# Kernel optimization log

Measured on AMD Instinct MI355X. Metric: run time of the kernel, lower is better.

The kernel has to match this reference:

```python
import jax, jax.numpy as jnp
import numpy as np

HEADS = 16
DK = 64
THETA = 10000.0


def _rope(x, cos, sin):
    # x: (B, S, H, dk) -> rotate consecutive pairs as complex numbers
    xr = x.reshape(*x.shape[:-1], -1, 2)
    a, b = xr[..., 0], xr[..., 1]
    c = cos[None, :, None, :]  # (1, S, 1, dk//2)
    s = sin[None, :, None, :]
    out = jnp.stack([a * c - b * s, a * s + b * c], axis=-1)
    return out.reshape(x.shape)


def setup_inputs() -> dict:
    key = jax.random.key(0)
    ks = jax.random.split(key, 5)
    B, S, D = 4, 2048, 1024
    x = jax.random.normal(ks[0], (B, S, D), dtype=jnp.float32)
    scale = 1.0 / np.sqrt(D).astype(np.float32)
    Wq = jax.random.normal(ks[1], (D, D), dtype=jnp.float32) * scale
    Wk = jax.random.normal(ks[2], (D, D), dtype=jnp.float32) * scale
    Wv = jax.random.normal(ks[3], (D, D), dtype=jnp.float32) * scale
    Wo = jax.random.normal(ks[4], (D, D), dtype=jnp.float32) * scale
    # freqs_cis = exp(i * t * theta^{-2j/dk}), represented as cos/sin
    t = jnp.arange(S, dtype=jnp.float32)
    inv_freq = 1.0 / (THETA ** (jnp.arange(0, DK, 2, dtype=jnp.float32) / DK))
    ang = t[:, None] * inv_freq[None, :]  # (S, dk//2)
    return {"in_features": x, "freqs_cos": jnp.cos(ang), "freqs_sin": jnp.sin(ang),
            "Wq": Wq, "Wk": Wk, "Wv": Wv, "Wo": Wo}


def reference(in_features, freqs_cos, freqs_sin, Wq, Wk, Wv, Wo):
    B, S, D = in_features.shape
    H = HEADS
    dk = D // H
    # Linear projections (torch Linear: x @ W.T)
    q = (in_features @ Wq.T).reshape(B, S, H, dk)
    k = (in_features @ Wk.T).reshape(B, S, H, dk)
    v = (in_features @ Wv.T).reshape(B, S, H, dk)
    q = _rope(q, freqs_cos, freqs_sin)
    k = _rope(k, freqs_cos, freqs_sin)
    scale = 1.0 / jnp.sqrt(jnp.asarray(dk, dtype=q.dtype))
    scores = jnp.einsum("bqhd,bkhd->bhqk", q, k) * scale
    mask = jnp.tril(jnp.ones((S, S), dtype=bool))
    scores = jnp.where(mask[None, None, :, :], scores, -jnp.inf)
    attn = jax.nn.softmax(scores, axis=-1)
    out = jnp.einsum("bhqk,bkhd->bqhd", attn, v).reshape(B, S, D)
    return out @ Wo.T
```

## Files before the change

kernel.cpp:

```cpp
#include <hip/hip_runtime.h>
#include <hip/hip_bf16.h>

typedef __attribute__((ext_vector_type(8))) __bf16 bf16x8;
typedef __attribute__((ext_vector_type(4))) __bf16 bf16x4;
typedef __attribute__((ext_vector_type(4))) float f32x4;
typedef __attribute__((ext_vector_type(2))) unsigned int u32x2;

static __device__ __forceinline__ f32x4 mfma_bf16(bf16x8 a, bf16x8 b, f32x4 c) {
  return __builtin_amdgcn_mfma_f32_16x16x32_bf16(a, b, c, 0, 0, 0);
}

static __device__ __forceinline__ void gload_lds16(const void* g, void* l) {
  __builtin_amdgcn_global_load_lds(
      (__attribute__((address_space(1))) unsigned int*)g,
      (__attribute__((address_space(3))) unsigned int*)l, 16, 0, 0);
}

static __device__ __forceinline__ unsigned int cvt_pk_bf16(float lo, float hi) {
  unsigned int r;
  asm volatile("v_cvt_pk_bf16_f32 %0, %1, %2" : "=v"(r) : "v"(lo), "v"(hi));
  return r;
}

__global__ void cvt_bf16(const float* __restrict__ in, __bf16* __restrict__ out, int n4) {
  int i = blockIdx.x * blockDim.x + threadIdx.x;
  if (i >= n4) return;
  f32x4 v = ((const f32x4*)in)[i];
  bf16x4 o;
#pragma unroll
  for (int k = 0; k < 4; ++k) o[k] = (__bf16)v[k];
  ((bf16x4*)out)[i] = o;
}

__global__ void cvt_w4(const float* __restrict__ w0, const float* __restrict__ w1,
                       const float* __restrict__ w2, const float* __restrict__ w3,
                       __bf16* __restrict__ o0, __bf16* __restrict__ o1,
                       __bf16* __restrict__ o2, __bf16* __restrict__ o3) {
  const float* in; __bf16* out;
  switch (blockIdx.y) {
    case 0: in = w0; out = o0; break;
    case 1: in = w1; out = o1; break;
    case 2: in = w2; out = o2; break;
    default: in = w3; out = o3; break;
  }
  int i = blockIdx.x * blockDim.x + threadIdx.x;
  f32x4 v = ((const f32x4*)in)[i];
  bf16x4 o;
#pragma unroll
  for (int k = 0; k < 4; ++k) o[k] = (__bf16)v[k];
  ((bf16x4*)out)[i] = o;
}

template <int MODE>
__global__ __launch_bounds__(512, 1)
void gemm256(const __bf16* __restrict__ A, const __bf16* __restrict__ W,
             void* __restrict__ outp,
             const float* __restrict__ fcos, const float* __restrict__ fsin) {
  constexpr int K = 1024;
  constexpr int NT = K / 64;
  extern __shared__ __align__(16) __bf16 dynlds[];
  __bf16* Al = dynlds;
  __bf16* Bl = dynlds + 49152;

  const int t = threadIdx.x;
  const int lane = t & 63, wave = t >> 6;
  const int g = lane >> 4, ln = lane & 15;
  const int wm = wave >> 1, wn = wave & 1;
  const int lin = blockIdx.x + blockIdx.y * 8;
  const int bm = (lin & 7) + 8 * ((lin >> 3) & 3);
  const int bn = lin >> 5;

  f32x4 acc[4][4] = {};

  const int srow8 = t >> 3;
  const int scole = (((t & 7) ^ ((t >> 3) & 7)) << 3);
  const __bf16* Ag = A + (size_t)(bm * 256 + srow8) * K + scole;
  const __bf16* Wg = W + (size_t)(bn * 128 + srow8) * K + scole;

#define ISSUE_A(kt, slot)                                                   \
  {                                                                         \
    const int k0 = (kt) * 64;                                               \
    __bf16* d = Al + (slot) * 16384 + t * 8;                                \
    gload_lds16(Ag + k0, d);                                                \
    gload_lds16(Ag + (size_t)64 * K + k0, d + 4096);                        \
    gload_lds16(Ag + (size_t)128 * K + k0, d + 8192);                       \
    gload_lds16(Ag + (size_t)192 * K + k0, d + 12288);                      \
  }
#define ISSUE_B(kt, slot)                                                   \
  {                                                                         \
    const int k0 = (kt) * 64;                                               \
    __bf16* d = Bl + (slot) * 8192 + t * 8;                                 \
    gload_lds16(Wg + k0, d);                                                \
    gload_lds16(Wg + (size_t)64 * K + k0, d + 4096);                        \
  }

  const int axr = ln & 7;
  int aoff[4], boff[4];
#pragma unroll
  for (int i = 0; i < 4; ++i) aoff[i] = (wm * 64 + i * 16 + ln) * 64;
#pragma unroll
  for (int j = 0; j < 4; ++j) boff[j] = (wn * 64 + j * 16 + ln) * 64;

  ISSUE_B(0, 0);
  ISSUE_A(0, 0);
  ISSUE_A(1, 1);
  asm volatile("s_waitcnt vmcnt(4)" ::: "memory");
  __builtin_amdgcn_s_barrier();

  int sa = 0;
  for (int tt = 0; tt < NT; ++tt) {
    const __bf16* Ab = Al + sa * 16384;
    const __bf16* Bb = Bl + (tt & 1) * 8192;
    bf16x8 af[4], bf[4];

#pragma unroll
    for (int i = 0; i < 4; ++i)
      af[i] = *(const bf16x8*)(Ab + aoff[i] + ((g ^ axr) << 3));
#pragma unroll
    for (int j = 0; j < 4; ++j)
      bf[j] = *(const bf16x8*)(Bb + boff[j] + ((g ^ axr) << 3));
    if (tt + 1 < NT) ISSUE_B(tt + 1, (tt + 1) & 1);
    if (tt + 2 < NT) ISSUE_A(tt + 2, sa == 0 ? 2 : sa - 1);
    __builtin_amdgcn_s_barrier();
    asm volatile("s_waitcnt lgkmcnt(0)" ::: "memory");
    __builtin_amdgcn_sched_barrier(0);
    __builtin_amdgcn_s_setprio(1);
#pragma unroll
    for (int i = 0; i < 4; ++i)
#pragma unroll
      for (int j = 0; j < 4; ++j)
        acc[i][j] = mfma_bf16(af[i], bf[j], acc[i][j]);
    __builtin_amdgcn_s_setprio(0);
    __builtin_amdgcn_s_barrier();

#pragma unroll
    for (int i = 0; i < 4; ++i)
      af[i] = *(const bf16x8*)(Ab + aoff[i] + (((4 | g) ^ axr) << 3));
#pragma unroll
    for (int j = 0; j < 4; ++j)
      bf[j] = *(const bf16x8*)(Bb + boff[j] + (((4 | g) ^ axr) << 3));
    if (tt < NT - 2) { asm volatile("s_waitcnt vmcnt(4)" ::: "memory"); }
    else             { asm volatile("s_waitcnt vmcnt(0)" ::: "memory"); }
    __builtin_amdgcn_s_barrier();
    asm volatile("s_waitcnt lgkmcnt(0)" ::: "memory");
    __builtin_amdgcn_sched_barrier(0);
    __builtin_amdgcn_s_setprio(1);
#pragma unroll
    for (int i = 0; i < 4; ++i)
#pragma unroll
      for (int j = 0; j < 4; ++j)
        acc[i][j] = mfma_bf16(af[i], bf[j], acc[i][j]);
    __builtin_amdgcn_s_setprio(0);
    __builtin_amdgcn_s_barrier();

    sa = (sa == 2) ? 0 : sa + 1;
  }
#undef ISSUE_A
#undef ISSUE_B

#pragma unroll
  for (int i = 0; i < 4; ++i) {
    const int mbase = bm * 256 + wm * 64 + i * 16 + g * 4;
#pragma unroll
    for (int j = 0; j < 4; ++j) {
      const int col = bn * 128 + wn * 64 + j * 16 + ln;
      if constexpr (MODE == 0 || MODE == 1) {
        const int fi = (col & 63) >> 1;
        const bool odd = (col & 1) != 0;
        __bf16* O = (__bf16*)outp;
#pragma unroll
        for (int r = 0; r < 4; ++r) {
          const int row = mbase + r;
          const int tok = row & 2047;
          const float cs = fcos[tok * 32 + fi];
          const float sn = fsin[tok * 32 + fi];
          const float own = acc[i][j][r];
          const float oth = __shfl_xor(own, 1);
          float val = own * cs + (odd ? oth * sn : -oth * sn);
          if constexpr (MODE == 0) val *= 0.1803368802f;
          O[(size_t)row * 1024 + col] = (__bf16)val;
        }
      } else if constexpr (MODE == 2) {
        __bf16* O = (__bf16*)outp;
        const int bb = mbase >> 11;
        const int tok = mbase & 2047;
        bf16x4 pk;
#pragma unroll
        for (int r = 0; r < 4; ++r) pk[r] = (__bf16)acc[i][j][r];
        *(bf16x4*)(O + ((size_t)(bb * 1024 + col)) * 2048 + tok) = pk;
      } else {
        float* O = (float*)outp;
#pragma unroll
        for (int r = 0; r < 4; ++r)
          O[(size_t)(mbase + r) * 1024 + col] = acc[i][j][r];
      }
    }
  }
}

__global__ __launch_bounds__(512, 4)
void attn_fwd(const __bf16* __restrict__ Q, const __bf16* __restrict__ Kk,
              const __bf16* __restrict__ Vt, __bf16* __restrict__ U) {
  constexpr int S = 2048;
  __shared__ __align__(16) __bf16 Klds[2][2 * 64 * 32];
  __shared__ __align__(16) __bf16 Vlds[2][2 * 64 * 32];
  __shared__ __align__(16) unsigned int Plds[8][16 * 36];

  const int t = threadIdx.x;
  const int lane = t & 63, wave = t >> 6;
  const int g = lane >> 4, ln = lane & 15;
  const int lin = blockIdx.x + blockIdx.y * 8;
  const int bh = (lin & 7) * 8 + ((lin >> 3) & 7);
  const int qt = lin >> 6;
  const int b = bh >> 4, h = bh & 15;
  const int q0s[2] = {qt * 128, (15 - qt) * 128};
  const int nts[2] = {2 * qt + 2, 32 - 2 * qt};

  bf16x8 qf[2][2];
#pragma unroll
  for (int s2 = 0; s2 < 2; ++s2) {
    const __bf16* Qb = Q + ((size_t)(b * S + q0s[s2] + wave * 16 + ln)) * 1024 + h * 64;
    qf[s2][0] = *(const bf16x8*)(Qb + g * 8);
    qf[s2][1] = *(const bf16x8*)(Qb + 32 + g * 8);
  }

  f32x4 o[2][4] = {};
  float mrow[2], lrow[2];
#pragma unroll
  for (int s2 = 0; s2 < 2; ++s2) { mrow[s2] = -3.0e38f; lrow[s2] = 0.f; }

  const int half = t >> 8;
  const int srow = (t >> 2) & 63;
  const int scol = (t & 3) * 8;
  const __bf16* Kg = Kk + ((size_t)(b * S + srow)) * 1024 + h * 64 + half * 32 + scol;
  const __bf16* Vg = Vt + ((size_t)(b * 1024 + h * 64 + srow)) * 2048 + half * 32 + scol;
  const int nt = nts[1];

  gload_lds16(Kg, (__bf16*)Klds[0] + t * 8);
  gload_lds16(Vg, (__bf16*)Vlds[0] + t * 8);
  __syncthreads();

  for (int kt = 0; kt < nt; ++kt) {
    const int cur = kt & 1;
    if (kt + 1 < nt) {
      const size_t kv1 = (size_t)(kt + 1) * 64;
      gload_lds16(Kg + kv1 * 1024, (__bf16*)Klds[cur ^ 1] + t * 8);
      gload_lds16(Vg + kv1, (__bf16*)Vlds[cur ^ 1] + t * 8);
    }
    const int kv0 = kt * 64;

#pragma unroll
    for (int s2 = 0; s2 < 2; ++s2) {
      if (kt >= nts[s2]) continue;

      f32x4 sa[4] = {};
      __builtin_amdgcn_s_setprio(1);
#pragma unroll
      for (int s = 0; s < 2; ++s) {
#pragma unroll
        for (int c = 0; c < 4; ++c) {
          bf16x8 kf = *(const bf16x8*)(Klds[cur] + s * 2048 + (c * 16 + ln) * 32 + g * 8);
          sa[c] = mfma_bf16(kf, qf[s2][s], sa[c]);
        }
      }
      __builtin_amdgcn_s_setprio(0);

      const int rfbase = q0s[s2] + wave * 16;
      const int rq = rfbase + ln;
      if (kv0 + 63 > rfbase) {
#pragma unroll
        for (int c = 0; c < 4; ++c)
#pragma unroll
          for (int r = 0; r < 4; ++r)
            if (kv0 + c * 16 + g * 4 + r > rq) sa[c][r] = -1e30f;
      }

      const float a0 = fmaxf(fmaxf(sa[0][0], sa[0][1]), sa[0][2]);
      const float a1 = fmaxf(fmaxf(sa[0][3], sa[1][0]), sa[1][1]);
      const float a2 = fmaxf(fmaxf(sa[1][2], sa[1][3]), sa[2][0]);
      const float a3 = fmaxf(fmaxf(sa[2][1], sa[2][2]), sa[2][3]);
      const float a4 = fmaxf(fmaxf(sa[3][0], sa[3][1]), sa[3][2]);
      const float b0 = fmaxf(fmaxf(a0, a1), a2);
      const float b1 = fmaxf(fmaxf(a3, a4), sa[3][3]);
      float pm = fmaxf(b0, b1);

      if (__any(pm > mrow[s2] + 8.f)) {
        pm = fmaxf(pm, __shfl_xor(pm, 16));
        pm = fmaxf(pm, __shfl_xor(pm, 32));
        const float mn = fmaxf(mrow[s2], pm);
        const float alpha = exp2f(mrow[s2] - mn);
        mrow[s2] = mn;
        lrow[s2] *= alpha;
#pragma unroll
        for (int c2 = 0; c2 < 4; ++c2)
#pragma unroll
          for (int r = 0; r < 4; ++r) o[s2][c2][r] *= alpha;
      }

      float p[4][4];
#pragma unroll
      for (int c = 0; c < 4; ++c)
#pragma unroll
        for (int r = 0; r < 4; ++r) p[c][r] = exp2f(sa[c][r] - mrow[s2]);

      float ts[8];
#pragma unroll
      for (int i = 0; i < 8; ++i) ts[i] = p[i >> 2][i & 3] + p[2 + (i >> 2)][i & 3];
#pragma unroll
      for (int st = 4; st >= 1; st >>= 1)
#pragma unroll
        for (int i = 0; i < st; ++i) ts[i] += ts[i + st];
      float rs = ts[0];
      rs += __shfl_xor(rs, 16);
      rs += __shfl_xor(rs, 32);
      lrow[s2] += rs;

      unsigned int* Pw = Plds[wave] + ln * 36;
#pragma unroll
      for (int c = 0; c < 4; ++c) {
        u32x2 w;
        w[0] = cvt_pk_bf16(p[c][0], p[c][1]);
        w[1] = cvt_pk_bf16(p[c][2], p[c][3]);
        *(u32x2*)(Pw + 8 * c + 2 * g) = w;
      }

      __builtin_amdgcn_s_setprio(1);
#pragma unroll
      for (int sh = 0; sh < 2; ++sh) {
        bf16x8 pb = *(const bf16x8*)((const __bf16*)(Plds[wave]) + ln * 72 + sh * 32 + g * 8);
#pragma unroll
        for (int c2 = 0; c2 < 4; ++c2) {
          bf16x8 vf = *(const bf16x8*)(Vlds[cur] + sh * 2048 + (c2 * 16 + ln) * 32 + g * 8);
          o[s2][c2] = mfma_bf16(vf, pb, o[s2][c2]);
        }
      }
      __builtin_amdgcn_s_setprio(0);
    }
    __syncthreads();
  }

#pragma unroll
  for (int s2 = 0; s2 < 2; ++s2) {
    const float rl = 1.0f / lrow[s2];
    __bf16* Ub = U + ((size_t)(b * S + q0s[s2] + wave * 16 + ln)) * 1024 + h * 64;
#pragma unroll
    for (int c2 = 0; c2 < 4; ++c2) {
      bf16x4 pk4;
#pragma unroll
      for (int r = 0; r < 4; ++r) pk4[r] = (__bf16)(o[s2][c2][r] * rl);
      *(bf16x4*)(Ub + 16 * c2 + 4 * g) = pk4;
    }
  }
}

extern "C" void kernel_launch(void* const* d_in, const int* in_sizes, int n_in,
                              void* d_out, int out_size, void* d_ws, size_t ws_size,
                              hipStream_t stream) {
  const float* x    = (const float*)d_in[0];
  const float* fcos = (const float*)d_in[1];
  const float* fsin = (const float*)d_in[2];
  const float* Wq   = (const float*)d_in[3];
  const float* Wk   = (const float*)d_in[4];
  const float* Wv   = (const float*)d_in[5];
  const float* Wo   = (const float*)d_in[6];

  char* ws = (char*)d_ws;
  __bf16* xb  = (__bf16*)(ws);
  __bf16* Wqb = (__bf16*)(ws + (16u << 20));
  __bf16* Wkb = (__bf16*)(ws + (18u << 20));
  __bf16* Wvb = (__bf16*)(ws + (20u << 20));
  __bf16* Wob = (__bf16*)(ws + (22u << 20));
  __bf16* Qb  = (__bf16*)(ws + (24u << 20));
  __bf16* Kb  = (__bf16*)(ws + (40u << 20));
  __bf16* Vtb = (__bf16*)(ws + (56u << 20));
  __bf16* Ub  = xb;

  cvt_bf16<<<8192, 256, 0, stream>>>(x, xb, 8192 * 1024 / 4);
  cvt_w4<<<dim3(1024, 4), 256, 0, stream>>>(Wq, Wk, Wv, Wo, Wqb, Wkb, Wvb, Wob);

  dim3 gg(8, 32);
  const size_t lds = 131072;
  gemm256<0><<<gg, 512, lds, stream>>>(xb, Wqb, Qb,  fcos, fsin);
  gemm256<1><<<gg, 512, lds, stream>>>(xb, Wkb, Kb,  fcos, fsin);
  gemm256<2><<<gg, 512, lds, stream>>>(xb, Wvb, Vtb, nullptr, nullptr);
  attn_fwd<<<dim3(8, 64), 512, 0, stream>>>(Qb, Kb, Vtb, Ub);
  gemm256<3><<<gg, 512, lds, stream>>>(Ub, Wob, d_out, nullptr, nullptr);
}
```

Baseline: 187.3 us.

## Merge Q/K/V projection GEMMs into one launch and interleave attention score MFMAs

Replaces three separate projection GEMM launches with one 768-block grid that picks Wq/Wk/Wv per block, so the grid fills the GPU better and launch gaps and tails are removed. In attention, the two query sub-tiles now share each K fragment load for their QK MFMAs, and softmax/PV is factored into a helper with separate P buffers per sub-tile. The cost is runtime branching on mode in the epilogue and doubled P LDS, which may affect occupancy or register pressure.

```diff
diff --git a/kernel.cpp b/kernel.cpp
--- a/kernel.cpp
+++ b/kernel.cpp
@@ -51,32 +51,6 @@
   ((bf16x4*)out)[i] = o;
 }
 
-template <int MODE>
-__global__ __launch_bounds__(512, 1)
-void gemm256(const __bf16* __restrict__ A, const __bf16* __restrict__ W,
-             void* __restrict__ outp,
-             const float* __restrict__ fcos, const float* __restrict__ fsin) {
-  constexpr int K = 1024;
-  constexpr int NT = K / 64;
-  extern __shared__ __align__(16) __bf16 dynlds[];
-  __bf16* Al = dynlds;
-  __bf16* Bl = dynlds + 49152;
-
-  const int t = threadIdx.x;
-  const int lane = t & 63, wave = t >> 6;
-  const int g = lane >> 4, ln = lane & 15;
-  const int wm = wave >> 1, wn = wave & 1;
-  const int lin = blockIdx.x + blockIdx.y * 8;
-  const int bm = (lin & 7) + 8 * ((lin >> 3) & 3);
-  const int bn = lin >> 5;
-
-  f32x4 acc[4][4] = {};
-
-  const int srow8 = t >> 3;
-  const int scole = (((t & 7) ^ ((t >> 3) & 7)) << 3);
-  const __bf16* Ag = A + (size_t)(bm * 256 + srow8) * K + scole;
-  const __bf16* Wg = W + (size_t)(bn * 128 + srow8) * K + scole;
-
 #define ISSUE_A(kt, slot)                                                   \
   {                                                                         \
     const int k0 = (kt) * 64;                                               \
@@ -94,69 +68,82 @@
     gload_lds16(Wg + (size_t)64 * K + k0, d + 4096);                        \
   }
 
-  const int axr = ln & 7;
-  int aoff[4], boff[4];
-#pragma unroll
-  for (int i = 0; i < 4; ++i) aoff[i] = (wm * 64 + i * 16 + ln) * 64;
-#pragma unroll
-  for (int j = 0; j < 4; ++j) boff[j] = (wn * 64 + j * 16 + ln) * 64;
-
-  ISSUE_B(0, 0);
-  ISSUE_A(0, 0);
-  ISSUE_A(1, 1);
-  asm volatile("s_waitcnt vmcnt(4)" ::: "memory");
-  __builtin_amdgcn_s_barrier();
-
-  int sa = 0;
-  for (int tt = 0; tt < NT; ++tt) {
-    const __bf16* Ab = Al + sa * 16384;
-    const __bf16* Bb = Bl + (tt & 1) * 8192;
-    bf16x8 af[4], bf[4];
-
-#pragma unroll
-    for (int i = 0; i < 4; ++i)
-      af[i] = *(const bf16x8*)(Ab + aoff[i] + ((g ^ axr) << 3));
-#pragma unroll
-    for (int j = 0; j < 4; ++j)
-      bf[j] = *(const bf16x8*)(Bb + boff[j] + ((g ^ axr) << 3));
-    if (tt + 1 < NT) ISSUE_B(tt + 1, (tt + 1) & 1);
-    if (tt + 2 < NT) ISSUE_A(tt + 2, sa == 0 ? 2 : sa - 1);
-    __builtin_amdgcn_s_barrier();
-    asm volatile("s_waitcnt lgkmcnt(0)" ::: "memory");
-    __builtin_amdgcn_sched_barrier(0);
-    __builtin_amdgcn_s_setprio(1);
-#pragma unroll
-    for (int i = 0; i < 4; ++i)
-#pragma unroll
-      for (int j = 0; j < 4; ++j)
-        acc[i][j] = mfma_bf16(af[i], bf[j], acc[i][j]);
-    __builtin_amdgcn_s_setprio(0);
-    __builtin_amdgcn_s_barrier();
-
-#pragma unroll
-    for (int i = 0; i < 4; ++i)
-      af[i] = *(const bf16x8*)(Ab + aoff[i] + (((4 | g) ^ axr) << 3));
-#pragma unroll
-    for (int j = 0; j < 4; ++j)
-      bf[j] = *(const bf16x8*)(Bb + boff[j] + (((4 | g) ^ axr) << 3));
-    if (tt < NT - 2) { asm volatile("s_waitcnt vmcnt(4)" ::: "memory"); }
-    else             { asm volatile("s_waitcnt vmcnt(0)" ::: "memory"); }
-    __builtin_amdgcn_s_barrier();
-    asm volatile("s_waitcnt lgkmcnt(0)" ::: "memory");
-    __builtin_amdgcn_sched_barrier(0);
-    __builtin_amdgcn_s_setprio(1);
-#pragma unroll
-    for (int i = 0; i < 4; ++i)
-#pragma unroll
-      for (int j = 0; j < 4; ++j)
-        acc[i][j] = mfma_bf16(af[i], bf[j], acc[i][j]);
-    __builtin_amdgcn_s_setprio(0);
-    __builtin_amdgcn_s_barrier();
-
-    sa = (sa == 2) ? 0 : sa + 1;
-  }
-#undef ISSUE_A
-#undef ISSUE_B
+#define GEMM_PIPELINE                                                       \
+  constexpr int K = 1024;                                                   \
+  constexpr int NT = K / 64;                                                \
+  extern __shared__ __align__(16) __bf16 dynlds[];                          \
+  __bf16* Al = dynlds;                                                      \
+  __bf16* Bl = dynlds + 49152;                                              \
+  const int t = threadIdx.x;                                                \
+  const int lane = t & 63, wave = t >> 6;                                   \
+  const int g = lane >> 4, ln = lane & 15;                                  \
+  const int wm = wave >> 1, wn = wave & 1;                                  \
+  f32x4 acc[4][4] = {};                                                     \
+  const int srow8 = t >> 3;                                                 \
+  const int scole = (((t & 7) ^ ((t >> 3) & 7)) << 3);                      \
+  const __bf16* Ag = A + (size_t)(bm * 256 + srow8) * K + scole;            \
+  const __bf16* Wg = W + (size_t)(bn * 128 + srow8) * K + scole;            \
+  const int axr = ln & 7;                                                   \
+  int aoff[4], boff[4];                                                     \
+  _Pragma("unroll") for (int i = 0; i < 4; ++i)                             \
+    aoff[i] = (wm * 64 + i * 16 + ln) * 64;                                 \
+  _Pragma("unroll") for (int j = 0; j < 4; ++j)                             \
+    boff[j] = (wn * 64 + j * 16 + ln) * 64;                                 \
+  ISSUE_B(0, 0); ISSUE_A(0, 0); ISSUE_A(1, 1);                              \
+  asm volatile("s_waitcnt vmcnt(4)" ::: "memory");                          \
+  __builtin_amdgcn_s_barrier();                                             \
+  int sa = 0;                                                               \
+  for (int tt = 0; tt < NT; ++tt) {                                         \
+    const __bf16* Ab = Al + sa * 16384;                                     \
+    const __bf16* Bb = Bl + (tt & 1) * 8192;                                \
+    bf16x8 af[4], bf[4];                                                    \
+    _Pragma("unroll") for (int i = 0; i < 4; ++i)                           \
+      af[i] = *(const bf16x8*)(Ab + aoff[i] + ((g ^ axr) << 3));            \
+    _Pragma("unroll") for (int j = 0; j < 4; ++j)                           \
+      bf[j] = *(const bf16x8*)(Bb + boff[j] + ((g ^ axr) << 3));            \
+    if (tt + 1 < NT) ISSUE_B(tt + 1, (tt + 1) & 1);                         \
+    if (tt + 2 < NT) ISSUE_A(tt + 2, sa == 0 ? 2 : sa - 1);                 \
+    __builtin_amdgcn_s_barrier();                                           \
+    asm volatile("s_waitcnt lgkmcnt(0)" ::: "memory");                      \
+    __builtin_amdgcn_sched_barrier(0);                                      \
+    __builtin_amdgcn_s_setprio(1);                                          \
+    _Pragma("unroll") for (int i = 0; i < 4; ++i)                           \
+      _Pragma("unroll") for (int j = 0; j < 4; ++j)                         \
+        acc[i][j] = mfma_bf16(af[i], bf[j], acc[i][j]);                     \
+    __builtin_amdgcn_s_setprio(0);                                          \
+    __builtin_amdgcn_s_barrier();                                           \
+    _Pragma("unroll") for (int i = 0; i < 4; ++i)                           \
+      af[i] = *(const bf16x8*)(Ab + aoff[i] + (((4 | g) ^ axr) << 3));      \
+    _Pragma("unroll") for (int j = 0; j < 4; ++j)                           \
+      bf[j] = *(const bf16x8*)(Bb + boff[j] + (((4 | g) ^ axr) << 3));      \
+    if (tt < NT - 2) { asm volatile("s_waitcnt vmcnt(4)" ::: "memory"); }   \
+    else             { asm volatile("s_waitcnt vmcnt(0)" ::: "memory"); }   \
+    __builtin_amdgcn_s_barrier();                                           \
+    asm volatile("s_waitcnt lgkmcnt(0)" ::: "memory");                      \
+    __builtin_amdgcn_sched_barrier(0);                                      \
+    __builtin_amdgcn_s_setprio(1);                                          \
+    _Pragma("unroll") for (int i = 0; i < 4; ++i)                           \
+      _Pragma("unroll") for (int j = 0; j < 4; ++j)                         \
+        acc[i][j] = mfma_bf16(af[i], bf[j], acc[i][j]);                     \
+    __builtin_amdgcn_s_setprio(0);                                          \
+    __builtin_amdgcn_s_barrier();                                           \
+    sa = (sa == 2) ? 0 : sa + 1;                                            \
+  }
+
+__global__ __launch_bounds__(512, 1)
+void gemm_qkv(const __bf16* __restrict__ A,
+              const __bf16* __restrict__ Wqp, const __bf16* __restrict__ Wkp,
+              const __bf16* __restrict__ Wvp,
+              __bf16* __restrict__ Qo, __bf16* __restrict__ Ko,
+              __bf16* __restrict__ Vo,
+              const float* __restrict__ fcos, const float* __restrict__ fsin) {
+  const int lin = blockIdx.x + blockIdx.y * 24;
+  const int bm = (lin & 7) + 8 * ((lin >> 3) / 24);
+  const int bn3 = (lin >> 3) % 24;
+  const int mode = bn3 >> 3, bn = bn3 & 7;
+  const __bf16* W = (mode == 0) ? Wqp : (mode == 1) ? Wkp : Wvp;
+
+  GEMM_PIPELINE
 
 #pragma unroll
   for (int i = 0; i < 4; ++i) {
@@ -164,10 +151,11 @@
 #pragma unroll
     for (int j = 0; j < 4; ++j) {
       const int col = bn * 128 + wn * 64 + j * 16 + ln;
-      if constexpr (MODE == 0 || MODE == 1) {
+      if (mode < 2) {
         const int fi = (col & 63) >> 1;
         const bool odd = (col & 1) != 0;
-        __bf16* O = (__bf16*)outp;
+        __bf16* O = (mode == 0) ? Qo : Ko;
+        const float sc = (mode == 0) ? 0.1803368802f : 1.0f;
 #pragma unroll
         for (int r = 0; r < 4; ++r) {
           const int row = mbase + r;
@@ -176,26 +164,104 @@
           const float sn = fsin[tok * 32 + fi];
           const float own = acc[i][j][r];
           const float oth = __shfl_xor(own, 1);
-          float val = own * cs + (odd ? oth * sn : -oth * sn);
-          if constexpr (MODE == 0) val *= 0.1803368802f;
-          O[(size_t)row * 1024 + col] = (__bf16)val;
+          O[(size_t)row * 1024 + col] =
+              (__bf16)((own * cs + (odd ? oth * sn : -oth * sn)) * sc);
         }
-      } else if constexpr (MODE == 2) {
-        __bf16* O = (__bf16*)outp;
+      } else {
         const int bb = mbase >> 11;
         const int tok = mbase & 2047;
         bf16x4 pk;
 #pragma unroll
         for (int r = 0; r < 4; ++r) pk[r] = (__bf16)acc[i][j][r];
-        *(bf16x4*)(O + ((size_t)(bb * 1024 + col)) * 2048 + tok) = pk;
-      } else {
-        float* O = (float*)outp;
-#pragma unroll
-        for (int r = 0; r < 4; ++r)
-          O[(size_t)(mbase + r) * 1024 + col] = acc[i][j][r];
+        *(bf16x4*)(Vo + ((size_t)(bb * 1024 + col)) * 2048 + tok) = pk;
       }
     }
   }
+}
+
+__global__ __launch_bounds__(512, 1)
+void gemm_out(const __bf16* __restrict__ A, const __bf16* __restrict__ W,
+              float* __restrict__ outp) {
+  const int lin = blockIdx.x + blockIdx.y * 8;
+  const int bm = (lin & 7) + 8 * ((lin >> 3) & 3);
+  const int bn = lin >> 5;
+
+  GEMM_PIPELINE
+
+#pragma unroll
+  for (int i = 0; i < 4; ++i) {
+    const int mbase = bm * 256 + wm * 64 + i * 16 + g * 4;
+#pragma unroll
+    for (int j = 0; j < 4; ++j) {
+      const int col = bn * 128 + wn * 64 + j * 16 + ln;
+#pragma unroll
+      for (int r = 0; r < 4; ++r)
+        outp[(size_t)(mbase + r) * 1024 + col] = acc[i][j][r];
+    }
+  }
+}
+
+static __device__ __forceinline__ void sm_pack_pv(
+    f32x4* sa, float& m, float& l, f32x4* o,
+    unsigned int* Pw, const __bf16* Vb, const int g, const int ln) {
+  const float a0 = fmaxf(fmaxf(sa[0][0], sa[0][1]), sa[0][2]);
+  const float a1 = fmaxf(fmaxf(sa[0][3], sa[1][0]), sa[1][1]);
+  const float a2 = fmaxf(fmaxf(sa[1][2], sa[1][3]), sa[2][0]);
+  const float a3 = fmaxf(fmaxf(sa[2][1], sa[2][2]), sa[2][3]);
+  const float a4 = fmaxf(fmaxf(sa[3][0], sa[3][1]), sa[3][2]);
+  float pm = fmaxf(fmaxf(fmaxf(a0, a1), a2), fmaxf(fmaxf(a3, a4), sa[3][3]));
+
+  if (__any(pm > m + 8.f)) {
+    pm = fmaxf(pm, __shfl_xor(pm, 16));
+    pm = fmaxf(pm, __shfl_xor(pm, 32));
+    const float mn = fmaxf(m, pm);
+    const float alpha = exp2f(m - mn);
+    m = mn;
+    l *= alpha;
+#pragma unroll
+    for (int c2 = 0; c2 < 4; ++c2)
+#pragma unroll
+      for (int r = 0; r < 4; ++r) o[c2][r] *= alpha;
+  }
+
+  float p[4][4];
+#pragma unroll
+  for (int c = 0; c < 4; ++c)
+#pragma unroll
+    for (int r = 0; r < 4; ++r) p[c][r] = exp2f(sa[c][r] - m);
+
+  float ts[8];
+#pragma unroll
+  for (int i = 0; i < 8; ++i) ts[i] = p[i >> 2][i & 3] + p[2 + (i >> 2)][i & 3];
+#pragma unroll
+  for (int st = 4; st >= 1; st >>= 1)
+#pragma unroll
+    for (int i = 0; i < st; ++i) ts[i] += ts[i + st];
+  float rs = ts[0];
+  rs += __shfl_xor(rs, 16);
+  rs += __shfl_xor(rs, 32);
+  l += rs;
+
+  unsigned int* Pr = Pw + ln * 36;
+#pragma unroll
+  for (int c = 0; c < 4; ++c) {
+    u32x2 w;
+    w[0] = cvt_pk_bf16(p[c][0], p[c][1]);
+    w[1] = cvt_pk_bf16(p[c][2], p[c][3]);
+    *(u32x2*)(Pr + 8 * c + 2 * g) = w;
+  }
+
+  __builtin_amdgcn_s_setprio(1);
+#pragma unroll
+  for (int sh = 0; sh < 2; ++sh) {
+    bf16x8 pb = *(const bf16x8*)((const __bf16*)Pw + ln * 72 + sh * 32 + g * 8);
+#pragma unroll
+    for (int c2 = 0; c2 < 4; ++c2) {
+      bf16x8 vf = *(const bf16x8*)(Vb + sh * 2048 + (c2 * 16 + ln) * 32 + g * 8);
+      o[c2] = mfma_bf16(vf, pb, o[c2]);
+    }
+  }
+  __builtin_amdgcn_s_setprio(0);
 }
 
 __global__ __launch_bounds__(512, 4)
@@ -204,7 +270,7 @@
   constexpr int S = 2048;
   __shared__ __align__(16) __bf16 Klds[2][2 * 64 * 32];
   __shared__ __align__(16) __bf16 Vlds[2][2 * 64 * 32];
-  __shared__ __align__(16) unsigned int Plds[8][16 * 36];
+  __shared__ __align__(16) unsigned int Plds[2][8][16 * 36];
 
   const int t = threadIdx.x;
   const int lane = t & 63, wave = t >> 6;
@@ -249,92 +315,56 @@
     }
     const int kv0 = kt * 64;
 
-#pragma unroll
-    for (int s2 = 0; s2 < 2; ++s2) {
-      if (kt >= nts[s2]) continue;
-
-      f32x4 sa[4] = {};
+    if (kt < nts[0]) {
+      f32x4 sa0[4] = {}, sa1[4] = {};
       __builtin_amdgcn_s_setprio(1);
 #pragma unroll
       for (int s = 0; s < 2; ++s) {
 #pragma unroll
         for (int c = 0; c < 4; ++c) {
           bf16x8 kf = *(const bf16x8*)(Klds[cur] + s * 2048 + (c * 16 + ln) * 32 + g * 8);
-          sa[c] = mfma_bf16(kf, qf[s2][s], sa[c]);
+          sa0[c] = mfma_bf16(kf, qf[0][s], sa0[c]);
+          sa1[c] = mfma_bf16(kf, qf[1][s], sa1[c]);
         }
       }
       __builtin_amdgcn_s_setprio(0);
 
-      const int rfbase = q0s[s2] + wave * 16;
-      const int rq = rfbase + ln;
-      if (kv0 + 63 > rfbase) {
+      const int rfbase0 = q0s[0] + wave * 16;
+      const int rq0 = rfbase0 + ln;
+      if (kv0 + 63 > rfbase0) {
 #pragma unroll
         for (int c = 0; c < 4; ++c)
 #pragma unroll
           for (int r = 0; r < 4; ++r)
-            if (kv0 + c * 16 + g * 4 + r > rq) sa[c][r] = -1e30f;
+            if (kv0 + c * 16 + g * 4 + r > rq0) sa0[c][r] = -1e30f;
       }
 
-      const float a0 = fmaxf(fmaxf(sa[0][0], sa[0][1]), sa[0][2]);
-      const float a1 = fmaxf(fmaxf(sa[0][3], sa[1][0]), sa[1][1]);
-      const float a2 = fmaxf(fmaxf(sa[1][2], sa[1][3]), sa[2][0]);
-      const float a3 = fmaxf(fmaxf(sa[2][1], sa[2][2]), sa[2][3]);
-      const float a4 = fmaxf(fmaxf(sa[3][0], sa[3][1]), sa[3][2]);
-      const float b0 = fmaxf(fmaxf(a0, a1), a2);
-      const float b1 = fmaxf(fmaxf(a3, a4), sa[3][3]);
-      float pm = fmaxf(b0, b1);
-
-      if (__any(pm > mrow[s2] + 8.f)) {
-        pm = fmaxf(pm, __shfl_xor(pm, 16));
-        pm = fmaxf(pm, __shfl_xor(pm, 32));
-        const float mn = fmaxf(mrow[s2], pm);
-        const float alpha = exp2f(mrow[s2] - mn);
-        mrow[s2] = mn;
-        lrow[s2] *= alpha;
-#pragma unroll
-        for (int c2 = 0; c2 < 4; ++c2)
-#pragma unroll
-          for (int r = 0; r < 4; ++r) o[s2][c2][r] *= alpha;
-      }
-
-      float p[4][4];
-#pragma unroll
-      for (int c = 0; c < 4; ++c)
-#pragma unroll
-        for (int r = 0; r < 4; ++r) p[c][r] = exp2f(sa[c][r] - mrow[s2]);
-
-      float ts[8];
-#pragma unroll
-      for (int i = 0; i < 8; ++i) ts[i] = p[i >> 2][i & 3] + p[2 + (i >> 2)][i & 3];
-#pragma unroll
-      for (int st = 4; st >= 1; st >>= 1)
-#pragma unroll
-        for (int i = 0; i < st; ++i) ts[i] += ts[i + st];
-      float rs = ts[0];
-      rs += __shfl_xor(rs, 16);
-      rs += __shfl_xor(rs, 32);
-      lrow[s2] += rs;
-
-      unsigned int* Pw = Plds[wave] + ln * 36;
-#pragma unroll
-      for (int c = 0; c < 4; ++c) {
-        u32x2 w;
-        w[0] = cvt_pk_bf16(p[c][0], p[c][1]);
-        w[1] = cvt_pk_bf16(p[c][2], p[c][3]);
-        *(u32x2*)(Pw + 8 * c + 2 * g) = w;
-      }
-
+      sm_pack_pv(sa0, mrow[0], lrow[0], o[0], Plds[0][wave], Vlds[cur], g, ln);
+      sm_pack_pv(sa1, mrow[1], lrow[1], o[1], Plds[1][wave], Vlds[cur], g, ln);
+    } else {
+      f32x4 sa1[4] = {};
       __builtin_amdgcn_s_setprio(1);
 #pragma unroll
-      for (int sh = 0; sh < 2; ++sh) {
-        bf16x8 pb = *(const bf16x8*)((const __bf16*)(Plds[wave]) + ln * 72 + sh * 32 + g * 8);
-#pragma unroll
-        for (int c2 = 0; c2 < 4; ++c2) {
-          bf16x8 vf = *(const bf16x8*)(Vlds[cur] + sh * 2048 + (c2 * 16 + ln) * 32 + g * 8);
-          o[s2][c2] = mfma_bf16(vf, pb, o[s2][c2]);
+      for (int s = 0; s < 2; ++s) {
+#pragma unroll
+        for (int c = 0; c < 4; ++c) {
+          bf16x8 kf = *(const bf16x8*)(Klds[cur] + s * 2048 + (c * 16 + ln) * 32 + g * 8);
+          sa1[c] = mfma_bf16(kf, qf[1][s], sa1[c]);
         }
       }
       __builtin_amdgcn_s_setprio(0);
+
+      const int rfbase1 = q0s[1] + wave * 16;
+      const int rq1 = rfbase1 + ln;
+      if (kv0 + 63 > rfbase1) {
+#pragma unroll
+        for (int c = 0; c < 4; ++c)
+#pragma unroll
+          for (int r = 0; r < 4; ++r)
+            if (kv0 + c * 16 + g * 4 + r > rq1) sa1[c][r] = -1e30f;
+      }
+
+      sm_pack_pv(sa1, mrow[1], lrow[1], o[1], Plds[1][wave], Vlds[cur], g, ln);
     }
     __syncthreads();
   }
@@ -378,11 +408,9 @@
   cvt_bf16<<<8192, 256, 0, stream>>>(x, xb, 8192 * 1024 / 4);
   cvt_w4<<<dim3(1024, 4), 256, 0, stream>>>(Wq, Wk, Wv, Wo, Wqb, Wkb, Wvb, Wob);
 
-  dim3 gg(8, 32);
   const size_t lds = 131072;
-  gemm256<0><<<gg, 512, lds, stream>>>(xb, Wqb, Qb,  fcos, fsin);
-  gemm256<1><<<gg, 512, lds, stream>>>(xb, Wkb, Kb,  fcos, fsin);
-  gemm256<2><<<gg, 512, lds, stream>>>(xb, Wvb, Vtb, nullptr, nullptr);
+  gemm_qkv<<<dim3(24, 32), 512, lds, stream>>>(xb, Wqb, Wkb, Wvb, Qb, Kb, Vtb,
+                                               fcos, fsin);
   attn_fwd<<<dim3(8, 64), 512, 0, stream>>>(Qb, Kb, Vtb, Ub);
-  gemm256<3><<<gg, 512, lds, stream>>>(Ub, Wob, d_out, nullptr, nullptr);
-}
+  gemm_out<<<dim3(8, 32), 512, lds, stream>>>(Ub, Wob, (float*)d_out);
+}
```

After: 187.2 us. Within noise of the previous version (-0.0%).
